# Kernel tuning notes

Hardware: AMD Instinct MI355X
Metric: run time of the kernel (lower is better)

## Reference

```python
import jax, jax.numpy as jnp
import numpy as np

B, T, D, R, V = 32, 14, 1024, 4, 8192


def setup_inputs() -> dict:
    key = jax.random.key(0)
    k1, k2, k3, k4, k5 = jax.random.split(key, 5)
    input_embs = jax.random.normal(k1, (B, T, D), dtype=jnp.float32)
    label_ids = jax.random.randint(k2, (B, T), 0, V)
    w_alpha = jax.random.normal(k3, (D, R), dtype=jnp.float32)
    w_beta = jax.random.normal(k4, (D, R), dtype=jnp.float32)
    w_vocab = jax.random.normal(k5, (D, V * R * R), dtype=jnp.float32)
    return {"input_embs": input_embs, "label_ids": label_ids,
            "w_alpha": w_alpha, "w_beta": w_beta, "w_vocab": w_vocab}


def _tt_params(x, w_alpha, w_beta, w_vocab):
    b, t, d = x.shape
    r = w_alpha.shape[1]
    v = w_vocab.shape[1] // (r * r)
    xf = x.reshape(-1, d)
    alpha = jax.nn.sigmoid((xf @ w_alpha).reshape(b, t, r).mean(1)) + 0.001   # (B,R)
    beta = jax.nn.sigmoid((xf @ w_beta).reshape(b, t, r).mean(1)) + 0.001     # (B,R)
    core = jax.nn.sigmoid((xf @ w_vocab).reshape(b, t, r, v, r).mean(1)) * 0.01 + 0.001  # (B,R,V,R)
    return alpha, beta, core


def _chain_matmul(init, mats):
    # init: (B,R,R); mats: (n,B,R,R) -> sequential product init @ mats[0] @ ...
    def step(carry, m):
        return jnp.einsum('bik,bkj->bij', carry, m), None
    out, _ = jax.lax.scan(step, init, mats)
    return out


def reference(input_embs, label_ids, w_alpha, w_beta, w_vocab):
    alpha, beta, core = _tt_params(input_embs, w_alpha, w_beta, w_vocab)
    b, t = label_ids.shape
    # ---- _select: gather core slices at label indices, chain-multiply ----
    sel = core[jnp.arange(b)[:, None], :, label_ids, :]   # (B,T,R,R)
    sel = jnp.swapaxes(sel, 0, 1)                         # (T,B,R,R)
    chain = _chain_matmul(sel[0], sel[1:])                # (B,R,R)
    unnorm = jnp.einsum('bi,bij,bj->b', alpha, chain, beta)
    # ---- normalization: marginalized core multiplied T extra times (T+1 factors, as in source) ----
    cm = core.sum(axis=2)                                 # (B,R,R)
    cm_rep = jnp.broadcast_to(cm, (t,) + cm.shape)        # (T,B,R,R)
    nres = _chain_matmul(cm, cm_rep)                      # (B,R,R)
    norm = jnp.einsum('bi,bij,bj->b', alpha, nres, beta)
    probs = unnorm / norm + 0.001
    loss = -jnp.log(probs)
    return loss.mean()
```

## Files before the change

### kernel.cpp

```cpp
#include <hip/hip_runtime.h>
#include <cstdint>
#include <cstddef>

#define BB 32
#define TT 14
#define DD 1024
#define RR 4
#define VV 8192
#define NCOL (VV*RR*RR)

typedef float f32x16 __attribute__((ext_vector_type(16)));
typedef float f4 __attribute__((ext_vector_type(4)));
typedef short short8 __attribute__((ext_vector_type(8)));
typedef unsigned int uint;


__device__ __forceinline__ uint pack2(float a, float b) {
    return __builtin_amdgcn_perm(__builtin_bit_cast(uint, b),
                                 __builtin_bit_cast(uint, a), 0x07060302u);
}

__device__ __forceinline__ short8 packw(const float* w) {
    uint4 u = make_uint4(pack2(w[0], w[1]), pack2(w[2], w[3]),
                         pack2(w[4], w[5]), pack2(w[6], w[7]));
    return __builtin_bit_cast(short8, u);
}

__global__ __launch_bounds__(256) void k_prep_all(const float* __restrict__ in,
                                                  const float* __restrict__ wa,
                                                  const float* __restrict__ wb,
                                                  ushort* __restrict__ xfrag_us,
                                                  float* __restrict__ alpha,
                                                  float* __restrict__ beta,
                                                  float* __restrict__ cm) {
    __shared__ float xl[DD];
    const int b   = blockIdx.x;
    const int tid = threadIdx.x;
    const int d0  = tid * 4;

    f4 s4 = (f4){0.f, 0.f, 0.f, 0.f};
    #pragma unroll
    for (int t = 0; t < TT; ++t) {
        f4 v = *reinterpret_cast<const f4*>(&in[((b * TT + t) << 10) + d0]);
        s4 += v;
    }
    s4 *= (1.0f / TT);
    *reinterpret_cast<f4*>(&xl[d0]) = s4;

    if (b == 0) { cm[tid] = 0.f; cm[tid + 256] = 0.f; }

    {
        const int s  = d0 >> 4;
        const int h  = (d0 >> 3) & 1;
        const int j0 = d0 & 7;
        uint2 u;
        u.x = pack2(s4.x, s4.y);
        u.y = pack2(s4.z, s4.w);
        *reinterpret_cast<uint2*>(&xfrag_us[((s * 64 + b + 32 * h) << 3) + j0]) = u;
    }

    __syncthreads();

    const int wave = tid >> 6, lane = tid & 63;
    for (int p = wave; p < 8; p += 4) {
        const int r = p >> 1, sf = p & 1;
        const float* wm = sf ? wb : wa;
        float acc = 0.f;
        #pragma unroll
        for (int k = 0; k < 16; ++k) {
            int d = lane + 64 * k;
            acc += xl[d] * wm[d * RR + r];
        }
        #pragma unroll
        for (int m = 1; m < 64; m <<= 1) acc += __shfl_xor(acc, m);
        if (lane == 0) {
            float v = 1.0f / (1.0f + __expf(-acc)) + 0.001f;
            (sf ? beta : alpha)[b * RR + r] = v;
        }
    }
}

#define LOADW(DST, STEP)                                                      \
    _Pragma("unroll")                                                         \
    for (int j = 0; j < 8; ++j)                                               \
        DST[j] = wp[(size_t)((STEP) * 16 + j) * NCOL];

__global__ __launch_bounds__(256) void k_core(const float* __restrict__ wv,
                                              const uint4* __restrict__ xfrag,
                                              const int*   __restrict__ lab,
                                              float* __restrict__ cm,
                                              float* __restrict__ sel) {
    const int tid  = threadIdx.x;
    const int lane = tid & 63;
    const int wvid = tid >> 6;
    const int n0   = blockIdx.x * 128 + wvid * 32;
    const int n    = n0 + (lane & 31);
    const int ii   = n >> 15;
    const int jj   = n & 3;
    const int vv   = (n >> 2) & (VV - 1);

    __shared__ int   lds_lab[BB * TT];
    __shared__ float cm_blk[BB][4];

    for (int idx = tid; idx < BB * TT; idx += 256) lds_lab[idx] = lab[idx];
    if (tid < BB * 4) ((float*)cm_blk)[tid] = 0.f;
    __syncthreads();

    const float* wp = wv + (size_t)((lane >> 5) * 8) * NCOL + n;

    f32x16 acc;
    #pragma unroll
    for (int q = 0; q < 16; ++q) acc[q] = 0.f;

    float w0[8], w1[8], w2[8], w3[8];
    uint4 ax0, ax1, ax2, ax3;
    LOADW(w0, 0); ax0 = xfrag[lane];
    LOADW(w1, 1); ax1 = xfrag[64 + lane];

    #pragma unroll 1
    for (int s = 0; s < 64; s += 4) {
        LOADW(w2, s + 2); ax2 = xfrag[((s + 2) << 6) + lane];
        LOADW(w3, s + 3); ax3 = xfrag[((s + 3) << 6) + lane];
        acc = __builtin_amdgcn_mfma_f32_32x32x16_bf16(
                  __builtin_bit_cast(short8, ax0), packw(w0), acc, 0, 0, 0);
        acc = __builtin_amdgcn_mfma_f32_32x32x16_bf16(
                  __builtin_bit_cast(short8, ax1), packw(w1), acc, 0, 0, 0);
        if (s + 4 < 64) {
            LOADW(w0, s + 4); ax0 = xfrag[((s + 4) << 6) + lane];
            LOADW(w1, s + 5); ax1 = xfrag[((s + 5) << 6) + lane];
        }
        acc = __builtin_amdgcn_mfma_f32_32x32x16_bf16(
                  __builtin_bit_cast(short8, ax2), packw(w2), acc, 0, 0, 0);
        acc = __builtin_amdgcn_mfma_f32_32x32x16_bf16(
                  __builtin_bit_cast(short8, ax3), packw(w3), acc, 0, 0, 0);
    }

    #pragma unroll
    for (int r = 0; r < 16; ++r) {
        float c = 0.01f / (1.0f + __expf(-acc[r])) + 0.001f;
        const int b = (r & 3) + 8 * (r >> 2) + 4 * (lane >> 5);
        float sred = c;
        sred += __shfl_xor(sred, 4);
        sred += __shfl_xor(sred, 8);
        sred += __shfl_xor(sred, 16);
        if ((lane & 31) < 4) atomicAdd(&cm_blk[b][lane & 3], sred);
        #pragma unroll
        for (int t = 0; t < TT; ++t)
            if (lds_lab[b * TT + t] == vv)
                sel[(b * TT + t) * 16 + (ii << 2) + jj] = c;
    }
    __syncthreads();
    if (tid < BB * 4) {
        int b = tid >> 2, j = tid & 3;
        atomicAdd(&cm[b * 16 + (ii << 2) + j], ((float*)cm_blk)[tid]);
    }
}

__global__ __launch_bounds__(64) void k_final(const float* __restrict__ cm,
                                              const float* __restrict__ sel,
                                              const float* __restrict__ alpha,
                                              const float* __restrict__ beta,
                                              float* __restrict__ out) {
    __shared__ float ls[BB];
    int b = threadIdx.x;
    if (b < BB) {
        float ch[16], tmp[16];
        #pragma unroll
        for (int q = 0; q < 16; ++q) ch[q] = sel[(b * TT + 0) * 16 + q];
        for (int t = 1; t < TT; ++t) {
            const float* m = &sel[(b * TT + t) * 16];
            #pragma unroll
            for (int i2 = 0; i2 < 4; ++i2)
                #pragma unroll
                for (int j2 = 0; j2 < 4; ++j2) {
                    float s = 0.f;
                    #pragma unroll
                    for (int k = 0; k < 4; ++k) s += ch[i2*4+k] * m[k*4+j2];
                    tmp[i2*4+j2] = s;
                }
            #pragma unroll
            for (int q = 0; q < 16; ++q) ch[q] = tmp[q];
        }

        float M[16], P[16];
        #pragma unroll
        for (int q = 0; q < 16; ++q) { M[q] = cm[b*16+q]; P[q] = M[q]; }
        for (int t = 0; t < TT; ++t) {
            #pragma unroll
            for (int i2 = 0; i2 < 4; ++i2)
                #pragma unroll
                for (int j2 = 0; j2 < 4; ++j2) {
                    float s = 0.f;
                    #pragma unroll
                    for (int k = 0; k < 4; ++k) s += P[i2*4+k] * M[k*4+j2];
                    tmp[i2*4+j2] = s;
                }
            #pragma unroll
            for (int q = 0; q < 16; ++q) P[q] = tmp[q];
        }

        float a[4], be[4];
        #pragma unroll
        for (int r = 0; r < 4; ++r) { a[r] = alpha[b*4+r]; be[r] = beta[b*4+r]; }
        float un = 0.f, no = 0.f;
        #pragma unroll
        for (int i2 = 0; i2 < 4; ++i2)
            #pragma unroll
            for (int j2 = 0; j2 < 4; ++j2) {
                un += a[i2] * ch[i2*4+j2] * be[j2];
                no += a[i2] * P [i2*4+j2] * be[j2];
            }
        float prob = un / no + 0.001f;
        ls[b] = -logf(prob);
    }
    __syncthreads();
    if (threadIdx.x == 0) {
        float s = 0.f;
        for (int q = 0; q < BB; ++q) s += ls[q];
        out[0] = s / BB;
    }
}

extern "C" void kernel_launch(void* const* d_in, const int* in_sizes, int n_in,
                              void* d_out, int out_size, void* d_ws, size_t ws_size,
                              hipStream_t stream) {
    const float* in_embs = (const float*)d_in[0];
    const int*   lab     = (const int*)  d_in[1];
    const float* wa      = (const float*)d_in[2];
    const float* wb      = (const float*)d_in[3];
    const float* wv      = (const float*)d_in[4];

    float* ws    = (float*)d_ws;
    float* cm    = ws;
    float* sel   = ws + 512;
    float* alpha = ws + 7680;
    float* beta  = ws + 7808;
    uint4* xfrag = (uint4*)(ws + 7936);

    k_prep_all<<<32,   256, 0, stream>>>(in_embs, wa, wb, (ushort*)xfrag,
                                         alpha, beta, cm);
    k_core    <<<1024, 256, 0, stream>>>(wv, xfrag, lab, cm, sel);
    k_final   <<<1,    64,  0, stream>>>(cm, sel, alpha, beta, (float*)d_out);
}
```

Baseline: 127.0 us.

## Widen k_core tiles to 128 columns per wave with float4 nontemporal weight loads

Each wave now computes four 32x32 MFMA tiles (128 columns) and loads weights as 16-byte nontemporal vectors instead of scalar floats. The x fragment is reused across the four tiles, and the grid shrinks from 1024 to 256 blocks. The aim is to cut load instruction count and improve streaming of the 512MB weight matrix. In exchange, accumulator registers grow fourfold (64 floats per lane), which may lower occupancy on a memory-bound kernel. The reduction epilogue is rewritten to match the new column mapping.

```diff
diff --git a/kernel.cpp b/kernel.cpp
--- a/kernel.cpp
+++ b/kernel.cpp
@@ -80,10 +80,21 @@
     }
 }
 
-#define LOADW(DST, STEP)                                                      \
+#define LOADW4(DST, STEP)                                                     \
     _Pragma("unroll")                                                         \
     for (int j = 0; j < 8; ++j)                                               \
-        DST[j] = wp[(size_t)((STEP) * 16 + j) * NCOL];
+        DST[j] = __builtin_nontemporal_load(reinterpret_cast<const f4*>(      \
+            wp + (size_t)(16 * (STEP) + j) * NCOL));
+
+#define MFMA_T4(WB, AX)                                                       \
+    _Pragma("unroll")                                                         \
+    for (int tt = 0; tt < 4; ++tt) {                                          \
+        float fr[8];                                                          \
+        _Pragma("unroll")                                                     \
+        for (int j = 0; j < 8; ++j) fr[j] = WB[j][tt];                        \
+        acc[tt] = __builtin_amdgcn_mfma_f32_32x32x16_bf16(                    \
+            __builtin_bit_cast(short8, AX), packw(fr), acc[tt], 0, 0, 0);     \
+    }
 
 __global__ __launch_bounds__(256) void k_core(const float* __restrict__ wv,
                                               const uint4* __restrict__ xfrag,
@@ -92,62 +103,62 @@
                                               float* __restrict__ sel) {
     const int tid  = threadIdx.x;
     const int lane = tid & 63;
-    const int wvid = tid >> 6;
-    const int n0   = blockIdx.x * 128 + wvid * 32;
-    const int n    = n0 + (lane & 31);
-    const int ii   = n >> 15;
-    const int jj   = n & 3;
-    const int vv   = (n >> 2) & (VV - 1);
+    const int c    = lane & 31;
+    const int h    = lane >> 5;
+    const int w    = tid >> 6;
+    const int W    = blockIdx.x * 512 + w * 128;
+    const int ii   = W >> 15;
+    const int vb   = W >> 2;
 
     __shared__ int   lds_lab[BB * TT];
     __shared__ float cm_blk[BB][4];
 
+    const float* wp = wv + (size_t)(8 * h) * NCOL + W + 4 * c;
+
+    f32x16 acc[4];
+    #pragma unroll
+    for (int t = 0; t < 4; ++t)
+        #pragma unroll
+        for (int q = 0; q < 16; ++q) acc[t][q] = 0.f;
+
+    f4 wA[8], wB[8];
+    uint4 axA, axB;
+    LOADW4(wA, 0); axA = xfrag[lane];
+    LOADW4(wB, 1); axB = xfrag[64 + lane];
+
+    #pragma unroll 1
+    for (int s = 0; s < 62; s += 2) {
+        MFMA_T4(wA, axA);
+        LOADW4(wA, s + 2); axA = xfrag[((s + 2) << 6) + lane];
+        MFMA_T4(wB, axB);
+        LOADW4(wB, s + 3); axB = xfrag[((s + 3) << 6) + lane];
+    }
+    MFMA_T4(wA, axA);
+    MFMA_T4(wB, axB);
+
     for (int idx = tid; idx < BB * TT; idx += 256) lds_lab[idx] = lab[idx];
     if (tid < BB * 4) ((float*)cm_blk)[tid] = 0.f;
     __syncthreads();
 
-    const float* wp = wv + (size_t)((lane >> 5) * 8) * NCOL + n;
-
-    f32x16 acc;
+    const int vv = vb + c;
     #pragma unroll
-    for (int q = 0; q < 16; ++q) acc[q] = 0.f;
-
-    float w0[8], w1[8], w2[8], w3[8];
-    uint4 ax0, ax1, ax2, ax3;
-    LOADW(w0, 0); ax0 = xfrag[lane];
-    LOADW(w1, 1); ax1 = xfrag[64 + lane];
-
-    #pragma unroll 1
-    for (int s = 0; s < 64; s += 4) {
-        LOADW(w2, s + 2); ax2 = xfrag[((s + 2) << 6) + lane];
-        LOADW(w3, s + 3); ax3 = xfrag[((s + 3) << 6) + lane];
-        acc = __builtin_amdgcn_mfma_f32_32x32x16_bf16(
-                  __builtin_bit_cast(short8, ax0), packw(w0), acc, 0, 0, 0);
-        acc = __builtin_amdgcn_mfma_f32_32x32x16_bf16(
-                  __builtin_bit_cast(short8, ax1), packw(w1), acc, 0, 0, 0);
-        if (s + 4 < 64) {
-            LOADW(w0, s + 4); ax0 = xfrag[((s + 4) << 6) + lane];
-            LOADW(w1, s + 5); ax1 = xfrag[((s + 5) << 6) + lane];
-        }
-        acc = __builtin_amdgcn_mfma_f32_32x32x16_bf16(
-                  __builtin_bit_cast(short8, ax2), packw(w2), acc, 0, 0, 0);
-        acc = __builtin_amdgcn_mfma_f32_32x32x16_bf16(
-                  __builtin_bit_cast(short8, ax3), packw(w3), acc, 0, 0, 0);
-    }
-
-    #pragma unroll
-    for (int r = 0; r < 16; ++r) {
-        float c = 0.01f / (1.0f + __expf(-acc[r])) + 0.001f;
-        const int b = (r & 3) + 8 * (r >> 2) + 4 * (lane >> 5);
-        float sred = c;
-        sred += __shfl_xor(sred, 4);
-        sred += __shfl_xor(sred, 8);
-        sred += __shfl_xor(sred, 16);
-        if ((lane & 31) < 4) atomicAdd(&cm_blk[b][lane & 3], sred);
-        #pragma unroll
-        for (int t = 0; t < TT; ++t)
-            if (lds_lab[b * TT + t] == vv)
-                sel[(b * TT + t) * 16 + (ii << 2) + jj] = c;
+    for (int tt = 0; tt < 4; ++tt) {
+        #pragma unroll
+        for (int r = 0; r < 16; ++r) {
+            float cval = 0.01f / (1.0f + __expf(-acc[tt][r])) + 0.001f;
+            const int b = (r & 3) + 8 * (r >> 2) + 4 * h;
+            float sred = cval;
+            sred += __shfl_xor(sred, 1);
+            sred += __shfl_xor(sred, 2);
+            sred += __shfl_xor(sred, 4);
+            sred += __shfl_xor(sred, 8);
+            sred += __shfl_xor(sred, 16);
+            if (c == 0) atomicAdd(&cm_blk[b][tt], sred);
+            #pragma unroll
+            for (int t = 0; t < TT; ++t)
+                if (lds_lab[b * TT + t] == vv)
+                    sel[(b * TT + t) * 16 + (ii << 2) + tt] = cval;
+        }
     }
     __syncthreads();
     if (tid < BB * 4) {
@@ -237,8 +248,8 @@
     float* beta  = ws + 7808;
     uint4* xfrag = (uint4*)(ws + 7936);
 
-    k_prep_all<<<32,   256, 0, stream>>>(in_embs, wa, wb, (ushort*)xfrag,
-                                         alpha, beta, cm);
-    k_core    <<<1024, 256, 0, stream>>>(wv, xfrag, lab, cm, sel);
-    k_final   <<<1,    64,  0, stream>>>(cm, sel, alpha, beta, (float*)d_out);
-}
+    k_prep_all<<<32,  256, 0, stream>>>(in_embs, wa, wb, (ushort*)xfrag,
+                                        alpha, beta, cm);
+    k_core    <<<256, 256, 0, stream>>>(wv, xfrag, lab, cm, sel);
+    k_final   <<<1,   64,  0, stream>>>(cm, sel, alpha, beta, (float*)d_out);
+}
```

Measured after the change: 150.7 us. 1.19x slower.
